# Kernel optimization log

Measured on AMD Instinct MI355X. Metric: run time of the kernel, lower is better.

The kernel has to match this reference:

```python
import jax, jax.numpy as jnp
import numpy as np

BN_EPS = 1e-5


def setup_inputs() -> dict:
    key = jax.random.key(0)
    ks = jax.random.split(key, 4)
    B, C, N = 4, 256, 4096
    Cq = C // 4
    return {
        "input_embedding": jax.random.normal(ks[0], (B, C, N), dtype=jnp.float32),
        "w_qk": jax.random.normal(ks[1], (Cq, C), dtype=jnp.float32) * (1.0 / np.sqrt(C)),
        "w_v": jax.random.normal(ks[2], (C, C), dtype=jnp.float32) * (1.0 / np.sqrt(C)),
        "b_v": jnp.zeros((C,), dtype=jnp.float32),
        "w_trans": jax.random.normal(ks[3], (C, C), dtype=jnp.float32) * (1.0 / np.sqrt(C)),
        "b_trans": jnp.zeros((C,), dtype=jnp.float32),
        "bn_gamma": jnp.ones((C,), dtype=jnp.float32),
        "bn_beta": jnp.zeros((C,), dtype=jnp.float32),
        "bn_mean": jnp.zeros((C,), dtype=jnp.float32),
        "bn_var": jnp.ones((C,), dtype=jnp.float32),
    }


def reference(input_embedding, w_qk, w_v, b_v, w_trans, b_trans,
              bn_gamma, bn_beta, bn_mean, bn_var):
    x = input_embedding  # (B, C, N)
    # 1x1 conv1d == channel matmul. Q and K share the same weight (tied in __init__).
    Q = jnp.einsum("qc,bcn->bnq", w_qk, x)              # (B, N, C/4)
    K = jnp.einsum("qc,bcn->bqn", w_qk, x)              # (B, C/4, N)
    V = jnp.einsum("oc,bcn->bon", w_v, x) + b_v[None, :, None]  # (B, C, N)
    scores = jnp.einsum("bnq,bqm->bnm", Q, K)           # (B, N, N)
    attn = jax.nn.softmax(scores, axis=-1)              # row softmax (dim=-1)
    # column L1 renormalization (sum over dim=1)
    attn = attn / (1e-9 + jnp.sum(attn, axis=1, keepdims=True))
    new_features = jnp.einsum("bcn,bnm->bcm", V, attn)  # (B, C, N)
    # offset residual -> trans conv -> BN (inference form) -> ReLU
    y = jnp.einsum("oc,bcn->bon", w_trans, x - new_features) + b_trans[None, :, None]
    inv_std = jax.lax.rsqrt(bn_var + BN_EPS)
    y = (y - bn_mean[None, :, None]) * (bn_gamma * inv_std)[None, :, None] + bn_beta[None, :, None]
    return jax.nn.relu(y)
```

## Files before the change

kernel.cpp:

```cpp
#include <hip/hip_runtime.h>

#define BATCH 4
#define CCH 256
#define NN 4096
#define CQ 64

typedef __bf16 bf16;
typedef __bf16 bf16x4 __attribute__((ext_vector_type(4)));
typedef __bf16 bf16x8 __attribute__((ext_vector_type(8)));
typedef float f32x4 __attribute__((ext_vector_type(4)));

static __device__ __forceinline__ f32x4 mfma16(bf16x8 a, bf16x8 b, f32x4 c) {
  return __builtin_amdgcn_mfma_f32_16x16x32_bf16(a, b, c, 0, 0, 0);
}

__global__ __launch_bounds__(256) void prep_kernel(const float* __restrict__ w_qk,
                                                   const float* __restrict__ w_v,
                                                   const float* __restrict__ w_trans,
                                                   bf16* __restrict__ wkvb,
                                                   bf16* __restrict__ wtb) {
  int i = blockIdx.x * 256 + threadIdx.x;
  if (i < 320 * 256) {
    int r = i >> 8, c = i & 255;
    float v = (r < 64) ? w_qk[r * 256 + c] : w_v[(r - 64) * 256 + c];
    wkvb[i] = (bf16)v;
  }
  if (i < 256 * 256) wtb[i] = (bf16)w_trans[i];
}

__global__ __launch_bounds__(256) void transpose_kernel(const float* __restrict__ x,
                                                        bf16* __restrict__ xTb) {
  __shared__ float t[64][65];
  int b = blockIdx.z, c0 = blockIdx.y * 64, n0 = blockIdx.x * 64;
  int tx = threadIdx.x & 63, ty = threadIdx.x >> 6;
  const float* xp = x + ((size_t)b * CCH + c0) * NN + n0;
#pragma unroll
  for (int j = 0; j < 16; ++j) {
    int cl = ty * 16 + j;
    t[tx][cl] = xp[(size_t)cl * NN + tx];
  }
  __syncthreads();
  bf16* op = xTb + ((size_t)b * NN + n0) * CCH + c0;
#pragma unroll
  for (int j = 0; j < 16; ++j) {
    int nl = ty * 16 + j;
    op[(size_t)nl * CCH + tx] = (bf16)t[nl][tx];
  }
}

__global__ __launch_bounds__(256) void kv_kernel(const bf16* __restrict__ wkvb,
                                                 const bf16* __restrict__ xTb,
                                                 const float* __restrict__ b_v,
                                                 bf16* __restrict__ Knq,
                                                 bf16* __restrict__ V,
                                                 float* __restrict__ sq) {
  int b = blockIdx.z, chunk = blockIdx.y;
  int w = threadIdx.x >> 6, lane = threadIdx.x & 63, lg = lane >> 4, lr = lane & 15;
  int n0 = blockIdx.x * 256 + w * 64;
  int r0 = chunk * 64;
  f32x4 z = {0.f, 0.f, 0.f, 0.f};
  f32x4 acc[4][4];
#pragma unroll
  for (int i = 0; i < 4; ++i)
#pragma unroll
    for (int j = 0; j < 4; ++j) acc[i][j] = z;

  for (int ks = 0; ks < 8; ++ks) {
    bf16x8 af[4], bb[4];
#pragma unroll
    for (int t = 0; t < 4; ++t)
      af[t] = *(const bf16x8*)(wkvb + (size_t)(r0 + 16 * t + lr) * 256 + 32 * ks + 8 * lg);
#pragma unroll
    for (int t = 0; t < 4; ++t)
      bb[t] = *(const bf16x8*)(xTb + ((size_t)b * NN + n0 + 16 * t + lr) * CCH + 32 * ks + 8 * lg);
#pragma unroll
    for (int tc = 0; tc < 4; ++tc)
#pragma unroll
      for (int tn = 0; tn < 4; ++tn) acc[tc][tn] = mfma16(af[tc], bb[tn], acc[tc][tn]);
  }

  if (chunk == 0) {
    float sqn[4];
#pragma unroll
    for (int tn = 0; tn < 4; ++tn) {
      int n = n0 + 16 * tn + lr;
#pragma unroll
      for (int tc = 0; tc < 4; ++tc) {
        bf16x4 kb;
#pragma unroll
        for (int r = 0; r < 4; ++r) kb[r] = (bf16)acc[tc][tn][r];
        *(bf16x4*)(Knq + ((size_t)b * NN + n) * CQ + 16 * tc + lg * 4) = kb;
      }
      float s = 0.f;
#pragma unroll
      for (int tc = 0; tc < 4; ++tc)
#pragma unroll
        for (int r = 0; r < 4; ++r) s += acc[tc][tn][r] * acc[tc][tn][r];
      s += __shfl_xor(s, 16);
      s += __shfl_xor(s, 32);
      sqn[tn] = s;
    }
    if (lane < 16) {
#pragma unroll
      for (int tn = 0; tn < 4; ++tn)
        sq[(size_t)b * NN + n0 + 16 * tn + lane] = sqn[tn];
    }
  } else {
#pragma unroll
    for (int tc = 0; tc < 4; ++tc) {
      int c4 = (chunk - 1) * 64 + 16 * tc + lg * 4;
      f32x4 bv = *(const f32x4*)(b_v + c4);
#pragma unroll
      for (int tn = 0; tn < 4; ++tn) {
        int n = n0 + 16 * tn + lr;
#pragma unroll
        for (int r = 0; r < 4; ++r)
          V[((size_t)b * CCH + c4 + r) * NN + n] = (bf16)(acc[tc][tn][r] + bv[r]);
      }
    }
  }
}

__global__ __launch_bounds__(256) void rnorm_kernel(const bf16* __restrict__ Knq,
                                                    const float* __restrict__ sq,
                                                    float* __restrict__ invr) {
  int b = blockIdx.y, n0 = blockIdx.x * 64;
  int w = threadIdx.x >> 6, lane = threadIdx.x & 63, lg = lane >> 4, lr = lane & 15;
  const bf16* Kb = Knq + (size_t)b * NN * CQ;
  int nr = n0 + 16 * w;
  bf16x8 a0 = *(const bf16x8*)(Kb + (size_t)(nr + lr) * CQ + 8 * lg);
  bf16x8 a1 = *(const bf16x8*)(Kb + (size_t)(nr + lr) * CQ + 32 + 8 * lg);
  f32x4 sh = *(const f32x4*)(sq + (size_t)b * NN + nr + lg * 4);
  f32x4 z = {0.f, 0.f, 0.f, 0.f};
  f32x4 ls = z;
  for (int mt = 0; mt < NN; mt += 64) {
#pragma unroll
    for (int j = 0; j < 4; ++j) {
      int m0 = mt + 16 * j;
      bf16x8 b0 = *(const bf16x8*)(Kb + (size_t)(m0 + lr) * CQ + 8 * lg);
      bf16x8 b1 = *(const bf16x8*)(Kb + (size_t)(m0 + lr) * CQ + 32 + 8 * lg);
      f32x4 s = mfma16(a0, b0, z);
      s = mfma16(a1, b1, s);
#pragma unroll
      for (int r = 0; r < 4; ++r) ls[r] += __expf(s[r] - sh[r]);
    }
  }
#pragma unroll
  for (int d = 1; d < 16; d <<= 1)
#pragma unroll
    for (int r = 0; r < 4; ++r) ls[r] += __shfl_xor(ls[r], d);
  if (lr == 0) {
#pragma unroll
    for (int r = 0; r < 4; ++r)
      invr[(size_t)b * NN + nr + lg * 4 + r] = 1.0f / ls[r];
  }
}

__global__ __launch_bounds__(512) void pv_kernel(const bf16* __restrict__ Knq,
                                                 const bf16* __restrict__ V,
                                                 const float* __restrict__ sq,
                                                 const float* __restrict__ invr,
                                                 const bf16* __restrict__ xTb,
                                                 bf16* __restrict__ DTb) {
  __shared__ bf16 Plds[64][136];
  __shared__ float csl[8][64];
  __shared__ float csv[64];
  int b = blockIdx.y, m0 = blockIdx.x * 64;
  int w = threadIdx.x >> 6, lane = threadIdx.x & 63, lg = lane >> 4, lr = lane & 15;
  const bf16* Kb = Knq + (size_t)b * NN * CQ;
  const bf16* Vb = V + (size_t)b * CCH * NN;
  f32x4 z = {0.f, 0.f, 0.f, 0.f};

  bf16x8 bS[4][2];
#pragma unroll
  for (int tj = 0; tj < 4; ++tj) {
    bS[tj][0] = *(const bf16x8*)(Kb + (size_t)(m0 + 16 * tj + lr) * CQ + 8 * lg);
    bS[tj][1] = *(const bf16x8*)(Kb + (size_t)(m0 + 16 * tj + lr) * CQ + 32 + 8 * lg);
  }

  f32x4 acc[2][4];
#pragma unroll
  for (int i = 0; i < 2; ++i)
#pragma unroll
    for (int j = 0; j < 4; ++j) acc[i][j] = z;
  float cs[4] = {0.f, 0.f, 0.f, 0.f};

  for (int n0 = 0; n0 < NN; n0 += 128) {
    int nr = n0 + 16 * w;
    bf16x8 a0 = *(const bf16x8*)(Kb + (size_t)(nr + lr) * CQ + 8 * lg);
    bf16x8 a1 = *(const bf16x8*)(Kb + (size_t)(nr + lr) * CQ + 32 + 8 * lg);
    f32x4 sh = *(const f32x4*)(sq + (size_t)b * NN + nr + lg * 4);
    f32x4 ri = *(const f32x4*)(invr + (size_t)b * NN + nr + lg * 4);
#pragma unroll
    for (int tj = 0; tj < 4; ++tj) {
      f32x4 s = mfma16(a0, bS[tj][0], z);
      s = mfma16(a1, bS[tj][1], s);
      bf16x4 pb;
#pragma unroll
      for (int r = 0; r < 4; ++r) {
        float p = __expf(s[r] - sh[r]) * ri[r];
        cs[tj] += p;
        pb[r] = (bf16)p;
      }
      *(bf16x4*)&Plds[16 * tj + lr][16 * w + lg * 4] = pb;
    }
    __syncthreads();
#pragma unroll
    for (int ks = 0; ks < 4; ++ks) {
      bf16x8 bp[4];
#pragma unroll
      for (int tj = 0; tj < 4; ++tj)
        bp[tj] = *(const bf16x8*)&Plds[16 * tj + lr][32 * ks + 8 * lg];
#pragma unroll
      for (int tc = 0; tc < 2; ++tc) {
        bf16x8 av = *(const bf16x8*)(Vb + (size_t)(32 * w + 16 * tc + lr) * NN + n0 + 32 * ks + 8 * lg);
#pragma unroll
        for (int tj = 0; tj < 4; ++tj) acc[tc][tj] = mfma16(av, bp[tj], acc[tc][tj]);
      }
    }
    __syncthreads();
  }

#pragma unroll
  for (int tj = 0; tj < 4; ++tj) {
    cs[tj] += __shfl_xor(cs[tj], 16);
    cs[tj] += __shfl_xor(cs[tj], 32);
  }
  if (lane < 16) {
#pragma unroll
    for (int tj = 0; tj < 4; ++tj) csl[w][16 * tj + lane] = cs[tj];
  }
  __syncthreads();
  if (threadIdx.x < 64) {
    int t = threadIdx.x;
    float s = 0.f;
#pragma unroll
    for (int ww = 0; ww < 8; ++ww) s += csl[ww][t];
    csv[t] = 1.0f / (1e-9f + s);
  }
  __syncthreads();

#pragma unroll
  for (int tj = 0; tj < 4; ++tj) {
    int ml = 16 * tj + lr;
    int m = m0 + ml;
    float ci = csv[ml];
#pragma unroll
    for (int tc = 0; tc < 2; ++tc) {
      int c4 = 32 * w + 16 * tc + lg * 4;
      bf16x4 xv = *(const bf16x4*)(xTb + ((size_t)b * NN + m) * CCH + c4);
      bf16x4 dv;
#pragma unroll
      for (int r = 0; r < 4; ++r) dv[r] = (bf16)((float)xv[r] - acc[tc][tj][r] * ci);
      *(bf16x4*)(DTb + ((size_t)b * NN + m) * CCH + c4) = dv;
    }
  }
}

__global__ __launch_bounds__(256) void final_kernel(const bf16* __restrict__ wtb,
                                                    const bf16* __restrict__ DTb,
                                                    const float* __restrict__ b_trans,
                                                    const float* __restrict__ gamma,
                                                    const float* __restrict__ beta,
                                                    const float* __restrict__ mean,
                                                    const float* __restrict__ var,
                                                    float* __restrict__ out) {
  int b = blockIdx.y;
  int w = threadIdx.x >> 6, lane = threadIdx.x & 63, lg = lane >> 4, lr = lane & 15;
  int n0 = blockIdx.x * 64;
  f32x4 z = {0.f, 0.f, 0.f, 0.f};
  f32x4 acc[4][4];
#pragma unroll
  for (int i = 0; i < 4; ++i)
#pragma unroll
    for (int j = 0; j < 4; ++j) acc[i][j] = z;

  for (int ks = 0; ks < 8; ++ks) {
    bf16x8 a[4], bb[4];
#pragma unroll
    for (int t = 0; t < 4; ++t)
      a[t] = *(const bf16x8*)(wtb + (size_t)(64 * w + 16 * t + lr) * 256 + 32 * ks + 8 * lg);
#pragma unroll
    for (int t = 0; t < 4; ++t)
      bb[t] = *(const bf16x8*)(DTb + ((size_t)b * NN + n0 + 16 * t + lr) * CCH + 32 * ks + 8 * lg);
#pragma unroll
    for (int tc = 0; tc < 4; ++tc)
#pragma unroll
      for (int tn = 0; tn < 4; ++tn) acc[tc][tn] = mfma16(a[tc], bb[tn], acc[tc][tn]);
  }

#pragma unroll
  for (int tc = 0; tc < 4; ++tc) {
    int c4 = 64 * w + 16 * tc + lg * 4;
    f32x4 bt = *(const f32x4*)(b_trans + c4);
    f32x4 gm = *(const f32x4*)(gamma + c4);
    f32x4 be = *(const f32x4*)(beta + c4);
    f32x4 mn = *(const f32x4*)(mean + c4);
    f32x4 vr = *(const f32x4*)(var + c4);
    f32x4 sc, shv;
#pragma unroll
    for (int r = 0; r < 4; ++r) {
      sc[r] = gm[r] * rsqrtf(vr[r] + 1e-5f);
      shv[r] = be[r] - mn[r] * sc[r];
    }
#pragma unroll
    for (int tn = 0; tn < 4; ++tn) {
      int n = n0 + 16 * tn + lr;
#pragma unroll
      for (int r = 0; r < 4; ++r) {
        float y = (acc[tc][tn][r] + bt[r]) * sc[r] + shv[r];
        out[((size_t)b * CCH + c4 + r) * NN + n] = fmaxf(y, 0.0f);
      }
    }
  }
}

extern "C" void kernel_launch(void* const* d_in, const int* in_sizes, int n_in,
                              void* d_out, int out_size, void* d_ws, size_t ws_size,
                              hipStream_t stream) {
  const float* x = (const float*)d_in[0];
  const float* w_qk = (const float*)d_in[1];
  const float* w_v = (const float*)d_in[2];
  const float* b_v = (const float*)d_in[3];
  const float* w_trans = (const float*)d_in[4];
  const float* b_trans = (const float*)d_in[5];
  const float* gamma = (const float*)d_in[6];
  const float* beta = (const float*)d_in[7];
  const float* mean = (const float*)d_in[8];
  const float* var = (const float*)d_in[9];
  float* out = (float*)d_out;

  char* p = (char*)d_ws;
  bf16* wkvb = (bf16*)p; p += (size_t)320 * 256 * 2;
  bf16* wtb = (bf16*)p;  p += (size_t)256 * 256 * 2;
  bf16* xTb = (bf16*)p;  p += (size_t)BATCH * NN * CCH * 2;
  bf16* Knq = (bf16*)p;  p += (size_t)BATCH * NN * CQ * 2;
  bf16* V = (bf16*)p;    p += (size_t)BATCH * CCH * NN * 2;
  float* sq = (float*)p;   p += (size_t)BATCH * NN * 4;
  float* invr = (float*)p; p += (size_t)BATCH * NN * 4;
  bf16* DTb = (bf16*)p;  p += (size_t)BATCH * NN * CCH * 2;

  hipLaunchKernelGGL(prep_kernel, dim3(320), dim3(256), 0, stream, w_qk, w_v, w_trans, wkvb, wtb);
  hipLaunchKernelGGL(transpose_kernel, dim3(NN / 64, CCH / 64, BATCH), dim3(256), 0, stream, x, xTb);
  hipLaunchKernelGGL(kv_kernel, dim3(NN / 256, 5, BATCH), dim3(256), 0, stream, wkvb, xTb, b_v, Knq, V, sq);
  hipLaunchKernelGGL(rnorm_kernel, dim3(NN / 64, BATCH), dim3(256), 0, stream, Knq, sq, invr);
  hipLaunchKernelGGL(pv_kernel, dim3(NN / 64, BATCH), dim3(512), 0, stream, Knq, V, sq, invr, xTb, DTb);
  hipLaunchKernelGGL(final_kernel, dim3(NN / 64, BATCH), dim3(256), 0, stream, wtb, DTb, b_trans, gamma, beta, mean, var, out);
}
```

Before: 295.4 us.

## Double-buffer P tiles in pv_kernel, swizzle LDS, remap blocks to XCDs, split rnorm

pv_kernel now double-buffers the probability tile in shared memory. The next step's score/exp phase is computed while the current tile's V loads and PV MFMAs are issued, which leaves one barrier per iteration. The LDS layout drops padding in favour of an XOR swizzle, and block IDs are remapped so each XCD works on a single batch, aiming for better L2 reuse of K and V. rnorm_kernel uses 512 threads, splits the m range between two wave groups and combines the partial sums through shared memory, which doubles parallelism at the cost of more registers and LDS use.

```diff
diff --git a/kernel.cpp b/kernel.cpp
--- a/kernel.cpp
+++ b/kernel.cpp
@@ -121,19 +121,21 @@
   }
 }
 
-__global__ __launch_bounds__(256) void rnorm_kernel(const bf16* __restrict__ Knq,
+__global__ __launch_bounds__(512) void rnorm_kernel(const bf16* __restrict__ Knq,
                                                     const float* __restrict__ sq,
                                                     float* __restrict__ invr) {
+  __shared__ float lsl[8][16];
   int b = blockIdx.y, n0 = blockIdx.x * 64;
   int w = threadIdx.x >> 6, lane = threadIdx.x & 63, lg = lane >> 4, lr = lane & 15;
+  int sn = w & 3, mh = w >> 2;
   const bf16* Kb = Knq + (size_t)b * NN * CQ;
-  int nr = n0 + 16 * w;
+  int nr = n0 + 16 * sn;
   bf16x8 a0 = *(const bf16x8*)(Kb + (size_t)(nr + lr) * CQ + 8 * lg);
   bf16x8 a1 = *(const bf16x8*)(Kb + (size_t)(nr + lr) * CQ + 32 + 8 * lg);
   f32x4 sh = *(const f32x4*)(sq + (size_t)b * NN + nr + lg * 4);
   f32x4 z = {0.f, 0.f, 0.f, 0.f};
   f32x4 ls = z;
-  for (int mt = 0; mt < NN; mt += 64) {
+  for (int mt = mh * (NN / 2); mt < (mh + 1) * (NN / 2); mt += 64) {
 #pragma unroll
     for (int j = 0; j < 4; ++j) {
       int m0 = mt + 16 * j;
@@ -151,21 +153,30 @@
     for (int r = 0; r < 4; ++r) ls[r] += __shfl_xor(ls[r], d);
   if (lr == 0) {
 #pragma unroll
-    for (int r = 0; r < 4; ++r)
-      invr[(size_t)b * NN + nr + lg * 4 + r] = 1.0f / ls[r];
-  }
-}
-
+    for (int r = 0; r < 4; ++r) lsl[w][lg * 4 + r] = ls[r];
+  }
+  __syncthreads();
+  if (threadIdx.x < 64) {
+    int t = threadIdx.x;
+    float S = lsl[t >> 4][t & 15] + lsl[(t >> 4) + 4][t & 15];
+    invr[(size_t)b * NN + n0 + t] = 1.0f / S;
+  }
+}
+
+#define SWZ(row, colb) ((colb) ^ (((row)&7) << 4))
 __global__ __launch_bounds__(512) void pv_kernel(const bf16* __restrict__ Knq,
                                                  const bf16* __restrict__ V,
                                                  const float* __restrict__ sq,
                                                  const float* __restrict__ invr,
                                                  const bf16* __restrict__ xTb,
                                                  bf16* __restrict__ DTb) {
-  __shared__ bf16 Plds[64][136];
+  __shared__ bf16 P2[2][64][128];
   __shared__ float csl[8][64];
   __shared__ float csv[64];
-  int b = blockIdx.y, m0 = blockIdx.x * 64;
+  int lin = blockIdx.y * (NN / 64) + blockIdx.x;
+  int xcd = lin & 7, slot = lin >> 3;
+  int b = xcd >> 1;
+  int m0 = (((xcd & 1) << 5) | slot) * 64;
   int w = threadIdx.x >> 6, lane = threadIdx.x & 63, lg = lane >> 4, lr = lane & 15;
   const bf16* Kb = Knq + (size_t)b * NN * CQ;
   const bf16* Vb = V + (size_t)b * CCH * NN;
@@ -185,39 +196,52 @@
     for (int j = 0; j < 4; ++j) acc[i][j] = z;
   float cs[4] = {0.f, 0.f, 0.f, 0.f};
 
-  for (int n0 = 0; n0 < NN; n0 += 128) {
-    int nr = n0 + 16 * w;
-    bf16x8 a0 = *(const bf16x8*)(Kb + (size_t)(nr + lr) * CQ + 8 * lg);
-    bf16x8 a1 = *(const bf16x8*)(Kb + (size_t)(nr + lr) * CQ + 32 + 8 * lg);
-    f32x4 sh = *(const f32x4*)(sq + (size_t)b * NN + nr + lg * 4);
-    f32x4 ri = *(const f32x4*)(invr + (size_t)b * NN + nr + lg * 4);
-#pragma unroll
-    for (int tj = 0; tj < 4; ++tj) {
-      f32x4 s = mfma16(a0, bS[tj][0], z);
-      s = mfma16(a1, bS[tj][1], s);
-      bf16x4 pb;
-#pragma unroll
-      for (int r = 0; r < 4; ++r) {
-        float p = __expf(s[r] - sh[r]) * ri[r];
-        cs[tj] += p;
-        pb[r] = (bf16)p;
-      }
-      *(bf16x4*)&Plds[16 * tj + lr][16 * w + lg * 4] = pb;
-    }
-    __syncthreads();
-#pragma unroll
-    for (int ks = 0; ks < 4; ++ks) {
-      bf16x8 bp[4];
+#define S_PHASE(STEP, BUF)                                                          \
+  {                                                                                 \
+    int nr_ = (STEP) * 128 + 16 * w;                                                \
+    bf16x8 a0_ = *(const bf16x8*)(Kb + (size_t)(nr_ + lr) * CQ + 8 * lg);           \
+    bf16x8 a1_ = *(const bf16x8*)(Kb + (size_t)(nr_ + lr) * CQ + 32 + 8 * lg);      \
+    f32x4 sh_ = *(const f32x4*)(sq + (size_t)b * NN + nr_ + lg * 4);                \
+    f32x4 ri_ = *(const f32x4*)(invr + (size_t)b * NN + nr_ + lg * 4);              \
+    _Pragma("unroll") for (int tj = 0; tj < 4; ++tj) {                              \
+      f32x4 s4 = mfma16(a0_, bS[tj][0], z);                                         \
+      s4 = mfma16(a1_, bS[tj][1], s4);                                              \
+      bf16x4 pb;                                                                    \
+      _Pragma("unroll") for (int r = 0; r < 4; ++r) {                               \
+        float p_ = __expf(s4[r] - sh_[r]) * ri_[r];                                 \
+        cs[tj] += p_;                                                               \
+        pb[r] = (bf16)p_;                                                           \
+      }                                                                             \
+      *(bf16x4*)((char*)&P2[BUF][16 * tj + lr][0] + SWZ(lr, 2 * (16 * w + 4 * lg))) = pb; \
+    }                                                                               \
+  }
+
+  S_PHASE(0, 0);
+  __syncthreads();
+
+  for (int s = 0; s < NN / 128; ++s) {
+    int cur = s & 1;
+    int ns = s * 128;
+    bf16x8 bp[4][4];
+#pragma unroll
+    for (int ks = 0; ks < 4; ++ks)
 #pragma unroll
       for (int tj = 0; tj < 4; ++tj)
-        bp[tj] = *(const bf16x8*)&Plds[16 * tj + lr][32 * ks + 8 * lg];
-#pragma unroll
-      for (int tc = 0; tc < 2; ++tc) {
-        bf16x8 av = *(const bf16x8*)(Vb + (size_t)(32 * w + 16 * tc + lr) * NN + n0 + 32 * ks + 8 * lg);
-#pragma unroll
-        for (int tj = 0; tj < 4; ++tj) acc[tc][tj] = mfma16(av, bp[tj], acc[tc][tj]);
-      }
-    }
+        bp[ks][tj] = *(const bf16x8*)((char*)&P2[cur][16 * tj + lr][0] +
+                                      SWZ(16 * tj + lr, 2 * (32 * ks + 8 * lg)));
+    bf16x8 av[4][2];
+#pragma unroll
+    for (int ks = 0; ks < 4; ++ks)
+#pragma unroll
+      for (int tc = 0; tc < 2; ++tc)
+        av[ks][tc] = *(const bf16x8*)(Vb + (size_t)(32 * w + 16 * tc + lr) * NN + ns + 32 * ks + 8 * lg);
+    if (s + 1 < NN / 128) S_PHASE(s + 1, cur ^ 1);
+#pragma unroll
+    for (int ks = 0; ks < 4; ++ks)
+#pragma unroll
+      for (int tc = 0; tc < 2; ++tc)
+#pragma unroll
+        for (int tj = 0; tj < 4; ++tj) acc[tc][tj] = mfma16(av[ks][tc], bp[ks][tj], acc[tc][tj]);
     __syncthreads();
   }
 
@@ -343,7 +367,7 @@
   hipLaunchKernelGGL(prep_kernel, dim3(320), dim3(256), 0, stream, w_qk, w_v, w_trans, wkvb, wtb);
   hipLaunchKernelGGL(transpose_kernel, dim3(NN / 64, CCH / 64, BATCH), dim3(256), 0, stream, x, xTb);
   hipLaunchKernelGGL(kv_kernel, dim3(NN / 256, 5, BATCH), dim3(256), 0, stream, wkvb, xTb, b_v, Knq, V, sq);
-  hipLaunchKernelGGL(rnorm_kernel, dim3(NN / 64, BATCH), dim3(256), 0, stream, Knq, sq, invr);
+  hipLaunchKernelGGL(rnorm_kernel, dim3(NN / 64, BATCH), dim3(512), 0, stream, Knq, sq, invr);
   hipLaunchKernelGGL(pv_kernel, dim3(NN / 64, BATCH), dim3(512), 0, stream, Knq, V, sq, invr, xTb, DTb);
   hipLaunchKernelGGL(final_kernel, dim3(NN / 64, BATCH), dim3(256), 0, stream, wtb, DTb, b_trans, gamma, beta, mean, var, out);
 }
```

After: 287.6 us. -2.6%, faster.
